# Kernel optimization log

Hardware: AMD Instinct MI355X
Metric: run time of the kernel (lower is better)

Reference implementation:

```python
import jax, jax.numpy as jnp
import numpy as np

B, LQ, LK = 1, 2048, 2048
D, H, KVH, DH = 4096, 32, 8, 128
G = H // KVH  # head groups


def setup_inputs() -> dict:
    key = jax.random.key(0)
    ks = jax.random.split(key, 7)
    s = 0.02
    hidden_q = jax.random.normal(ks[0], (B, LQ, D), dtype=jnp.float32)
    hidden_kv = jax.random.normal(ks[1], (B, LK, D), dtype=jnp.float32)
    # causal boolean mask (batch, len_q, len_k)
    attention_mask = jnp.broadcast_to(jnp.tril(jnp.ones((LQ, LK), dtype=bool)), (B, LQ, LK))
    position_bias = jax.random.normal(ks[2], (H, LQ, LK), dtype=jnp.float32) * 0.1
    Wq = jax.random.normal(ks[3], (D, H * DH), dtype=jnp.float32) * s
    Wk = jax.random.normal(ks[4], (D, KVH * DH), dtype=jnp.float32) * s
    Wv = jax.random.normal(ks[5], (D, KVH * DH), dtype=jnp.float32) * s
    Wo = jax.random.normal(ks[6], (H * DH, D), dtype=jnp.float32) * s
    return {"hidden_q": hidden_q, "hidden_kv": hidden_kv,
            "attention_mask": attention_mask, "position_bias": position_bias,
            "Wq": Wq, "Wk": Wk, "Wv": Wv, "Wo": Wo}


def reference(hidden_q, hidden_kv, attention_mask, position_bias, Wq, Wk, Wv, Wo):
    inv4 = DH ** -0.25  # q and k each scaled by dim_head**-1/4
    q = (hidden_q @ Wq) * inv4            # [B, LQ, H*DH]
    k = (hidden_kv @ Wk) * inv4           # [B, LK, KVH*DH]
    v = hidden_kv @ Wv                     # [B, LK, KVH*DH]
    q = q.reshape(B, LQ, KVH, G, DH)       # group heads for GQA
    k = k.reshape(B, LK, KVH, DH)
    v = v.reshape(B, LK, KVH, DH)
    # score: [B, KVH, G, LQ, LK] -> [B, H, LQ, LK]
    score = jnp.einsum('bqkgd,blkd->bkgql', q, k).reshape(B, H, LQ, LK)
    score = score + position_bias[None]
    mask = attention_mask[:, None]         # [B, 1, LQ, LK]
    score = jnp.where(mask, score, -jnp.inf)
    p = jax.nn.softmax(score, axis=-1)
    p = jnp.where(mask, p, 0.0)
    out = jnp.einsum('bkgql,blkd->bqkgd', p.reshape(B, KVH, G, LQ, LK), v)
    out = out.reshape(B, LQ, H * DH) @ Wo  # [B, LQ, D]
    return out
```

## Files before the change

### kernel.cpp

```cpp
#include <hip/hip_runtime.h>
#include <hip/hip_bf16.h>
#include <cstdint>
#include <cstddef>

typedef __attribute__((ext_vector_type(4))) float f32x4;
typedef __attribute__((ext_vector_type(4))) short s16x4;
typedef __attribute__((ext_vector_type(8))) short s16x8;

#define SLQ 2048
#define SLK 2048
#define SNH 32
#define SDH 128

__device__ __forceinline__ short f2bf(float x) {
  unsigned u = __builtin_bit_cast(unsigned, x);
  u += 0x7FFF + ((u >> 16) & 1);
  return (short)(u >> 16);
}

__device__ __forceinline__ void gload_lds16(const void* g, const void* l) {
  __builtin_amdgcn_global_load_lds((const __attribute__((address_space(1))) void*)g,
                                   (__attribute__((address_space(3))) void*)l,
                                   16, 0, 0);
}

template<int CTRL>
__device__ __forceinline__ float dpp_f32(float x) {
  return __builtin_bit_cast(float, __builtin_amdgcn_update_dpp(
      0, __builtin_bit_cast(int, x), CTRL, 0xF, 0xF, true));
}
__device__ __forceinline__ float rowmax16(float x) {
  x = fmaxf(x, dpp_f32<0x128>(x));
  x = fmaxf(x, dpp_f32<0x124>(x));
  x = fmaxf(x, dpp_f32<0x122>(x));
  x = fmaxf(x, dpp_f32<0x121>(x));
  return x;
}
__device__ __forceinline__ float rowsum16(float x) {
  x += dpp_f32<0x128>(x);
  x += dpp_f32<0x124>(x);
  x += dpp_f32<0x122>(x);
  x += dpp_f32<0x121>(x);
  return x;
}

__global__ void convert_bf16(const float* __restrict__ in, short* __restrict__ out, int n4) {
  int i = blockIdx.x * 256 + threadIdx.x;
  if (i < n4) {
    f32x4 a = ((const f32x4*)in)[i];
    s16x4 b;
    b[0] = f2bf(a[0]); b[1] = f2bf(a[1]); b[2] = f2bf(a[2]); b[3] = f2bf(a[3]);
    ((s16x4*)out)[i] = b;
  }
}

__global__ void transpose_convert(const float* __restrict__ W, short* __restrict__ Wt,
                                  int K, int N) {
  __shared__ short T[64][68];
  const int tid = threadIdx.x;
  const int k0 = blockIdx.y * 64, n0 = blockIdx.x * 64;
  const int r = tid >> 4;
  const int c4 = (tid & 15) * 4;
#pragma unroll
  for (int i = 0; i < 4; ++i) {
    f32x4 a = *(const f32x4*)(W + (size_t)(k0 + r + i * 16) * N + n0 + c4);
#pragma unroll
    for (int j = 0; j < 4; ++j) T[c4 + j][r + i * 16] = f2bf(a[j]);
  }
  __syncthreads();
  const int rn = tid >> 3;
  const int c8 = (tid & 7) * 8;
#pragma unroll
  for (int i = 0; i < 2; ++i) {
    s16x4 v0 = *(const s16x4*)&T[rn + i * 32][c8];
    s16x4 v1 = *(const s16x4*)&T[rn + i * 32][c8 + 4];
    short* dst = Wt + (size_t)(n0 + rn + i * 32) * K + k0 + c8;
    *(s16x4*)dst = v0;
    *(s16x4*)(dst + 4) = v1;
  }
}

template<int CM>
__global__ __launch_bounds__(512, 1)
void gemm_big(const short* __restrict__ A, const short* __restrict__ Bt,
              void* __restrict__ Cv, float scale) {
  __shared__ short As[3][128 * 64];
  __shared__ short Bs[3][256 * 64];
  const int N = 4096, K = 4096;
  const int tid = threadIdx.x, lane = tid & 63, w = tid >> 6;
  const int l15 = lane & 15, lg = lane >> 4;
  const int wr = w >> 2, wc = w & 3;
  const int nbx = N >> 8;
  const int nwg = gridDim.x, b = blockIdx.x;
  const int wg = (b & 7) * (nwg >> 3) + (b >> 3);
  const int m0 = (wg / nbx) * 128, n0 = (wg % nbx) * 256;

  f32x4 acc[4][4];
#pragma unroll
  for (int a = 0; a < 4; ++a)
#pragma unroll
    for (int c = 0; c < 4; ++c)
      acc[a][c] = (f32x4){0.f, 0.f, 0.f, 0.f};

#define GSTAGE(T, BUF) do {                                                    \
    _Pragma("unroll") for (int i_ = 0; i_ < 2; ++i_) {                         \
      const int ci = i_ * 512 + tid, r_ = ci >> 3, c_ = ci & 7;                \
      gload_lds16(A + (size_t)(m0 + r_) * K + (T) * 64 + ((c_ ^ (r_ & 7)) * 8),\
                  (const short*)As[BUF] + ci * 8); }                           \
    _Pragma("unroll") for (int i_ = 0; i_ < 4; ++i_) {                         \
      const int ci = i_ * 512 + tid, r_ = ci >> 3, c_ = ci & 7;                \
      gload_lds16(Bt + (size_t)(n0 + r_) * K + (T) * 64 + ((c_ ^ (r_ & 7)) * 8),\
                  (const short*)Bs[BUF] + ci * 8); }                           \
  } while (0)

  const int NT = K >> 6;
  GSTAGE(0, 0); GSTAGE(1, 1); GSTAGE(2, 2);
  int buf = 0;
  for (int t = 0; t < NT; ++t) {
    if (t + 2 < NT)      asm volatile("s_waitcnt vmcnt(12)" ::: "memory");
    else if (t + 1 < NT) asm volatile("s_waitcnt vmcnt(6)" ::: "memory");
    else                 asm volatile("s_waitcnt vmcnt(0)" ::: "memory");
    __builtin_amdgcn_s_barrier();
    const short* Ab = As[buf];
    const short* Bb = Bs[buf];
    s16x8 af[2][4], bfv[2][4];
#pragma unroll
    for (int kk = 0; kk < 2; ++kk) {
#pragma unroll
      for (int mi = 0; mi < 4; ++mi) {
        const int r = wr * 64 + mi * 16 + l15;
        const int c = (kk * 4 + lg) ^ (r & 7);
        af[kk][mi] = *(const s16x8*)(Ab + (r * 8 + c) * 8);
      }
#pragma unroll
      for (int ni = 0; ni < 4; ++ni) {
        const int r = wc * 64 + ni * 16 + l15;
        const int c = (kk * 4 + lg) ^ (r & 7);
        bfv[kk][ni] = *(const s16x8*)(Bb + (r * 8 + c) * 8);
      }
    }
    __builtin_amdgcn_s_setprio(1);
#pragma unroll
    for (int kk = 0; kk < 2; ++kk)
#pragma unroll
      for (int mi = 0; mi < 4; ++mi)
#pragma unroll
        for (int ni = 0; ni < 4; ++ni)
          acc[mi][ni] = __builtin_amdgcn_mfma_f32_16x16x32_bf16(af[kk][mi], bfv[kk][ni], acc[mi][ni], 0, 0, 0);
    __builtin_amdgcn_s_setprio(0);
    __builtin_amdgcn_s_barrier();
    if (t + 3 < NT) GSTAGE(t + 3, buf);
    buf = (buf == 2) ? 0 : buf + 1;
  }
#undef GSTAGE
#pragma unroll
  for (int mi = 0; mi < 4; ++mi) {
#pragma unroll
    for (int ni = 0; ni < 4; ++ni) {
#pragma unroll
      for (int j = 0; j < 4; ++j) {
        const int rg = m0 + wr * 64 + mi * 16 + lg * 4 + j;
        const int cg = n0 + wc * 64 + ni * 16 + l15;
        const float vv = acc[mi][ni][j] * scale;
        if (CM == 0) ((short*)Cv)[(size_t)rg * N + cg] = f2bf(vv);
        else         ((float*)Cv)[(size_t)rg * N + cg] = vv;
      }
    }
  }
}

__global__ __launch_bounds__(256, 2)
void gemm_kv(const short* __restrict__ A, const short* __restrict__ Bt,
             short* __restrict__ kout, short* __restrict__ vTout, float inv4) {
  __shared__ short As[128][32];
  __shared__ short Bs[128][32];
  const int N = 2048, K = 4096;
  const int tid = threadIdx.x, lane = tid & 63, wid = tid >> 6;
  const int l15 = lane & 15, lg = lane >> 4;
  const int nbx = N >> 7;
  const int nwg = gridDim.x, b = blockIdx.x;
  const int wg = (b & 7) * (nwg >> 3) + (b >> 3);
  const int m0 = (wg / nbx) * 128, n0 = (wg % nbx) * 128;
  const int wm = (wid >> 1) * 64, wn = (wid & 1) * 64;

  f32x4 acc[4][4];
#pragma unroll
  for (int a = 0; a < 4; ++a)
#pragma unroll
    for (int c = 0; c < 4; ++c)
      acc[a][c] = (f32x4){0.f, 0.f, 0.f, 0.f};

  for (int k0 = 0; k0 < K; k0 += 32) {
#pragma unroll
    for (int i = 0; i < 2; ++i) {
      const int c = i * 256 + wid * 64 + lane;
      const int rr = c >> 2, hh = (c & 3) * 8;
      gload_lds16(A  + (size_t)(m0 + rr) * K + k0 + hh,
                  (const short*)As + (size_t)(i * 256 + wid * 64) * 8);
      gload_lds16(Bt + (size_t)(n0 + rr) * K + k0 + hh,
                  (const short*)Bs + (size_t)(i * 256 + wid * 64) * 8);
    }
    __syncthreads();
    s16x8 af[4], bf[4];
#pragma unroll
    for (int mi = 0; mi < 4; ++mi)
      af[mi] = *(const s16x8*)&As[wm + mi * 16 + l15][lg * 8];
#pragma unroll
    for (int ni = 0; ni < 4; ++ni)
      bf[ni] = *(const s16x8*)&Bs[wn + ni * 16 + l15][lg * 8];
#pragma unroll
    for (int mi = 0; mi < 4; ++mi)
#pragma unroll
      for (int ni = 0; ni < 4; ++ni)
        acc[mi][ni] = __builtin_amdgcn_mfma_f32_16x16x32_bf16(af[mi], bf[ni], acc[mi][ni], 0, 0, 0);
    __syncthreads();
  }
  if (n0 < 1024) {
#pragma unroll
    for (int mi = 0; mi < 4; ++mi)
#pragma unroll
      for (int ni = 0; ni < 4; ++ni)
#pragma unroll
        for (int j = 0; j < 4; ++j) {
          const int rg = m0 + wm + mi * 16 + lg * 4 + j;
          const int cg = n0 + wn + ni * 16 + l15;
          kout[(size_t)rg * 1024 + cg] = f2bf(acc[mi][ni][j] * inv4);
        }
  } else {
#pragma unroll
    for (int mi = 0; mi < 4; ++mi)
#pragma unroll
      for (int ni = 0; ni < 4; ++ni) {
        s16x4 wv;
#pragma unroll
        for (int j = 0; j < 4; ++j) wv[j] = f2bf(acc[mi][ni][j]);
        const int rg0 = m0 + wm + mi * 16 + lg * 4;
        const int cg = n0 + wn + ni * 16 + l15 - 1024;
        *(s16x4*)(vTout + (size_t)cg * 2048 + rg0) = wv;
      }
  }
}

__global__ __launch_bounds__(256, 2)
void attn_kernel(const short* __restrict__ q, const short* __restrict__ k,
                 const short* __restrict__ vT, const float* __restrict__ bias,
                 short* __restrict__ o) {
  __shared__ __align__(16) short Ks[64 * 128];
  __shared__ __align__(16) short Vs[2][128 * 64];
  __shared__ __align__(16) short Ps[4][16][72];
  const int tid = threadIdx.x, lane = tid & 63, w = tid >> 6;
  const int l15 = lane & 15, lg = lane >> 4;
  const int b = blockIdx.x;
  const int h = b & 31;
  const int qt = 31 - (b >> 5);
  const int kvh = h >> 2;
  const int nt = qt + 1;

#define STAGE_K(IT) do { const int kv0_ = (IT) * 64;                          \
    _Pragma("unroll") for (int i_ = 0; i_ < 4; ++i_) {                        \
      const int ci = i_ * 256 + tid, r_ = ci >> 4, c_ = ci & 15;              \
      gload_lds16(k + (size_t)(kv0_ + r_) * 1024 + kvh * 128 + ((c_ ^ (r_ & 7)) * 8), \
                  (const short*)Ks + ci * 8); } } while (0)

#define STAGE_V(IT, P) do { const int kv0_ = (IT) * 64;                       \
    _Pragma("unroll") for (int i_ = 0; i_ < 4; ++i_) {                        \
      const int ci = i_ * 256 + tid, r_ = ci >> 3, c_ = ci & 7;               \
      gload_lds16(vT + (size_t)(kvh * 128 + r_) * 2048 + kv0_ + ((c_ ^ (r_ & 7)) * 8), \
                  (const short*)Vs[P] + ci * 8); } } while (0)

  const int qrow0 = qt * 64 + w * 16 + lg * 4;

  float bb[4][4];
#define LOAD_BIAS(IT) do { const float* bp_ = bias + ((size_t)h * SLQ + qrow0) * SLK + (IT) * 64 + l15; \
    _Pragma("unroll") for (int ni_ = 0; ni_ < 4; ++ni_)                       \
      _Pragma("unroll") for (int j_ = 0; j_ < 4; ++j_)                        \
        bb[ni_][j_] = bp_[(size_t)j_ * SLK + ni_ * 16]; } while (0)

  s16x8 qf[4];
  {
    const short* qp = q + (size_t)(qt * 64 + w * 16 + l15) * (SNH * SDH) + h * SDH + lg * 8;
#pragma unroll
    for (int kk = 0; kk < 4; ++kk) qf[kk] = *(const s16x8*)(qp + kk * 32);
  }
  float mrow[4], lrow[4];
  f32x4 oacc[8];
#pragma unroll
  for (int j = 0; j < 4; ++j) { mrow[j] = -1e30f; lrow[j] = 0.f; }
#pragma unroll
  for (int nd = 0; nd < 8; ++nd) oacc[nd] = (f32x4){0.f, 0.f, 0.f, 0.f};

  STAGE_V(0, 0);
  STAGE_K(0);
  LOAD_BIAS(0);

  for (int it = 0; it < nt; ++it) {
    const int p = it & 1;
    const int kv0 = it * 64;
    asm volatile("s_waitcnt vmcnt(16)" ::: "memory");
    __builtin_amdgcn_s_barrier();
    if (it + 1 < nt) STAGE_V(it + 1, p ^ 1);
    f32x4 s[4];
    __builtin_amdgcn_s_setprio(1);
#pragma unroll
    for (int ni = 0; ni < 4; ++ni) {
      s[ni] = (f32x4){0.f, 0.f, 0.f, 0.f};
      const int r = ni * 16 + l15;
#pragma unroll
      for (int kk = 0; kk < 4; ++kk) {
        const int cc = kk * 4 + lg;
        s16x8 kf = *(const s16x8*)(Ks + (r * 16 + (cc ^ (r & 7))) * 8);
        s[ni] = __builtin_amdgcn_mfma_f32_16x16x32_bf16(qf[kk], kf, s[ni], 0, 0, 0);
      }
    }
    __builtin_amdgcn_s_setprio(0);
#pragma unroll
    for (int ni = 0; ni < 4; ++ni) {
#pragma unroll
      for (int j = 0; j < 4; ++j) {
        float sv = s[ni][j] + bb[ni][j];
        if (it == qt && kv0 + ni * 16 + l15 > qrow0 + j) sv = -1e30f;
        s[ni][j] = sv;
      }
    }
    float pmax[4];
#pragma unroll
    for (int j = 0; j < 4; ++j) {
      float mx = fmaxf(fmaxf(s[0][j], s[1][j]), fmaxf(s[2][j], s[3][j]));
      pmax[j] = rowmax16(mx);
    }
    bool need = (pmax[0] > mrow[0] + 8.f) | (pmax[1] > mrow[1] + 8.f) |
                (pmax[2] > mrow[2] + 8.f) | (pmax[3] > mrow[3] + 8.f);
    if (__any(need)) {
#pragma unroll
      for (int j = 0; j < 4; ++j) {
        const float mn = fmaxf(mrow[j], pmax[j]);
        const float fsj = __expf(mrow[j] - mn);
        mrow[j] = mn;
        lrow[j] *= fsj;
#pragma unroll
        for (int nd = 0; nd < 8; ++nd) oacc[nd][j] *= fsj;
      }
    }
    float ps[4] = {0.f, 0.f, 0.f, 0.f};
#pragma unroll
    for (int ni = 0; ni < 4; ++ni)
#pragma unroll
      for (int j = 0; j < 4; ++j) {
        const float pv = __expf(s[ni][j] - mrow[j]);
        s[ni][j] = pv;
        ps[j] += pv;
      }
#pragma unroll
    for (int j = 0; j < 4; ++j) lrow[j] += rowsum16(ps[j]);
    __builtin_amdgcn_s_barrier();
    if (it + 1 < nt) { STAGE_K(it + 1); LOAD_BIAS(it + 1); }
#pragma unroll
    for (int ni = 0; ni < 4; ++ni)
#pragma unroll
      for (int j = 0; j < 4; ++j)
        Ps[w][lg * 4 + j][ni * 16 + l15] = f2bf(s[ni][j]);
    __builtin_amdgcn_s_setprio(1);
#pragma unroll
    for (int kk2 = 0; kk2 < 2; ++kk2) {
      s16x8 pa = *(const s16x8*)&Ps[w][l15][kk2 * 32 + lg * 8];
#pragma unroll
      for (int nd = 0; nd < 8; ++nd) {
        const int r = nd * 16 + l15;
        const int cc = kk2 * 4 + lg;
        s16x8 vf = *(const s16x8*)(Vs[p] + (r * 8 + (cc ^ (r & 7))) * 8);
        oacc[nd] = __builtin_amdgcn_mfma_f32_16x16x32_bf16(pa, vf, oacc[nd], 0, 0, 0);
      }
    }
    __builtin_amdgcn_s_setprio(0);
  }
#undef STAGE_K
#undef STAGE_V
#undef LOAD_BIAS
#pragma unroll
  for (int j = 0; j < 4; ++j) {
    const float inv = 1.f / lrow[j];
    short* op = o + (size_t)(qrow0 + j) * (SNH * SDH) + h * SDH + l15;
#pragma unroll
    for (int nd = 0; nd < 8; ++nd)
      op[nd * 16] = f2bf(oacc[nd][j] * inv);
  }
}

extern "C" void kernel_launch(void* const* d_in, const int* in_sizes, int n_in,
                              void* d_out, int out_size, void* d_ws, size_t ws_size,
                              hipStream_t stream) {
  (void)in_sizes; (void)n_in; (void)out_size; (void)ws_size;
  const float* hq   = (const float*)d_in[0];
  const float* hkv  = (const float*)d_in[1];
  const float* bias = (const float*)d_in[3];
  const float* Wq   = (const float*)d_in[4];
  const float* Wk   = (const float*)d_in[5];
  const float* Wv   = (const float*)d_in[6];
  const float* Wo   = (const float*)d_in[7];

  short* ws = (short*)d_ws;
  const size_t MEG = 1048576;
  short* hqb  = ws;
  short* hkvb = ws + 8 * MEG;
  short* WT   = ws + 16 * MEG;
  short* WkvT = ws + 32 * MEG;
  short* qb   = ws + 40 * MEG;
  short* kb   = ws + 48 * MEG;
  short* vbT  = ws + 50 * MEG;
  short* ob   = hqb;

  const float inv4 = 0.29730177875068026f;

  convert_bf16<<<8192, 256, 0, stream>>>(hq,  hqb,  2097152);
  convert_bf16<<<8192, 256, 0, stream>>>(hkv, hkvb, 2097152);

  transpose_convert<<<dim3(64, 64), 256, 0, stream>>>(Wq, WT, 4096, 4096);
  gemm_big<0><<<256, 512, 0, stream>>>(hqb, WT, qb, inv4);

  transpose_convert<<<dim3(16, 64), 256, 0, stream>>>(Wk, WkvT, 4096, 1024);
  transpose_convert<<<dim3(16, 64), 256, 0, stream>>>(Wv, WkvT + (size_t)1024 * 4096, 4096, 1024);
  gemm_kv<<<256, 256, 0, stream>>>(hkvb, WkvT, kb, vbT, inv4);

  attn_kernel<<<1024, 256, 0, stream>>>(qb, kb, vbT, bias, ob);

  transpose_convert<<<dim3(64, 64), 256, 0, stream>>>(Wo, WT, 4096, 4096);
  gemm_big<1><<<256, 512, 0, stream>>>(ob, WT, (float*)d_out, 1.0f);
}
```

Baseline: 425.9 us.

## Double-buffer K tiles, use exp2 softmax, and merge conversion/transpose launches

The attention kernel now double-buffers K in LDS so the next K and V tiles are staged right after the first barrier. This removes the second barrier per iteration, and the bias load is moved earlier. Softmax switches to exp2: log2(e) is folded into the Q projection scale and applied to the bias with an FMA, and the rescale threshold is widened to match. On the host side, the two conversions are fused into one launch and the four weight transposes into one, cutting launch count. The cost is more LDS, which may affect occupancy, plus a separate Wo buffer.

```diff
diff --git a/kernel.cpp b/kernel.cpp
--- a/kernel.cpp
+++ b/kernel.cpp
@@ -11,6 +11,7 @@
 #define SLK 2048
 #define SNH 32
 #define SDH 128
+#define LOG2E 1.4426950408889634f
 
 __device__ __forceinline__ short f2bf(float x) {
   unsigned u = __builtin_bit_cast(unsigned, x);
@@ -44,21 +45,31 @@
   return x;
 }
 
-__global__ void convert_bf16(const float* __restrict__ in, short* __restrict__ out, int n4) {
-  int i = blockIdx.x * 256 + threadIdx.x;
-  if (i < n4) {
-    f32x4 a = ((const f32x4*)in)[i];
-    s16x4 b;
-    b[0] = f2bf(a[0]); b[1] = f2bf(a[1]); b[2] = f2bf(a[2]); b[3] = f2bf(a[3]);
-    ((s16x4*)out)[i] = b;
-  }
-}
-
-__global__ void transpose_convert(const float* __restrict__ W, short* __restrict__ Wt,
-                                  int K, int N) {
+__global__ void convert_bf16_2(const float* __restrict__ in0, short* __restrict__ out0,
+                               const float* __restrict__ in1, short* __restrict__ out1) {
+  const int i = blockIdx.x * 256 + threadIdx.x;
+  const float* in = blockIdx.y ? in1 : in0;
+  short* out = blockIdx.y ? out1 : out0;
+  f32x4 a = ((const f32x4*)in)[i];
+  s16x4 b;
+  b[0] = f2bf(a[0]); b[1] = f2bf(a[1]); b[2] = f2bf(a[2]); b[3] = f2bf(a[3]);
+  ((s16x4*)out)[i] = b;
+}
+
+__global__ void transpose_all(const float* __restrict__ Wq, const float* __restrict__ Wo,
+                              const float* __restrict__ Wk, const float* __restrict__ Wv,
+                              short* __restrict__ WqT, short* __restrict__ WoT,
+                              short* __restrict__ WkT, short* __restrict__ WvT) {
   __shared__ short T[64][68];
+  const int K = 4096;
+  int bx = blockIdx.x;
+  const float* W; short* Wt; int N;
+  if (bx < 64)       { W = Wq; Wt = WqT; N = 4096; }
+  else if (bx < 128) { W = Wo; Wt = WoT; N = 4096; bx -= 64; }
+  else if (bx < 144) { W = Wk; Wt = WkT; N = 1024; bx -= 128; }
+  else               { W = Wv; Wt = WvT; N = 1024; bx -= 144; }
   const int tid = threadIdx.x;
-  const int k0 = blockIdx.y * 64, n0 = blockIdx.x * 64;
+  const int k0 = blockIdx.y * 64, n0 = bx * 64;
   const int r = tid >> 4;
   const int c4 = (tid & 15) * 4;
 #pragma unroll
@@ -245,7 +256,7 @@
 void attn_kernel(const short* __restrict__ q, const short* __restrict__ k,
                  const short* __restrict__ vT, const float* __restrict__ bias,
                  short* __restrict__ o) {
-  __shared__ __align__(16) short Ks[64 * 128];
+  __shared__ __align__(16) short Ks[2][64 * 128];
   __shared__ __align__(16) short Vs[2][128 * 64];
   __shared__ __align__(16) short Ps[4][16][72];
   const int tid = threadIdx.x, lane = tid & 63, w = tid >> 6;
@@ -256,11 +267,11 @@
   const int kvh = h >> 2;
   const int nt = qt + 1;
 
-#define STAGE_K(IT) do { const int kv0_ = (IT) * 64;                          \
+#define STAGE_K(IT, P) do { const int kv0_ = (IT) * 64;                       \
     _Pragma("unroll") for (int i_ = 0; i_ < 4; ++i_) {                        \
       const int ci = i_ * 256 + tid, r_ = ci >> 4, c_ = ci & 15;              \
       gload_lds16(k + (size_t)(kv0_ + r_) * 1024 + kvh * 128 + ((c_ ^ (r_ & 7)) * 8), \
-                  (const short*)Ks + ci * 8); } } while (0)
+                  (const short*)Ks[P] + ci * 8); } } while (0)
 
 #define STAGE_V(IT, P) do { const int kv0_ = (IT) * 64;                       \
     _Pragma("unroll") for (int i_ = 0; i_ < 4; ++i_) {                        \
@@ -290,7 +301,7 @@
   for (int nd = 0; nd < 8; ++nd) oacc[nd] = (f32x4){0.f, 0.f, 0.f, 0.f};
 
   STAGE_V(0, 0);
-  STAGE_K(0);
+  STAGE_K(0, 0);
   LOAD_BIAS(0);
 
   for (int it = 0; it < nt; ++it) {
@@ -298,7 +309,7 @@
     const int kv0 = it * 64;
     asm volatile("s_waitcnt vmcnt(16)" ::: "memory");
     __builtin_amdgcn_s_barrier();
-    if (it + 1 < nt) STAGE_V(it + 1, p ^ 1);
+    if (it + 1 < nt) { STAGE_V(it + 1, p ^ 1); STAGE_K(it + 1, p ^ 1); }
     f32x4 s[4];
     __builtin_amdgcn_s_setprio(1);
 #pragma unroll
@@ -308,7 +319,7 @@
 #pragma unroll
       for (int kk = 0; kk < 4; ++kk) {
         const int cc = kk * 4 + lg;
-        s16x8 kf = *(const s16x8*)(Ks + (r * 16 + (cc ^ (r & 7))) * 8);
+        s16x8 kf = *(const s16x8*)(Ks[p] + (r * 16 + (cc ^ (r & 7))) * 8);
         s[ni] = __builtin_amdgcn_mfma_f32_16x16x32_bf16(qf[kk], kf, s[ni], 0, 0, 0);
       }
     }
@@ -317,24 +328,25 @@
     for (int ni = 0; ni < 4; ++ni) {
 #pragma unroll
       for (int j = 0; j < 4; ++j) {
-        float sv = s[ni][j] + bb[ni][j];
+        float sv = fmaf(bb[ni][j], LOG2E, s[ni][j]);
         if (it == qt && kv0 + ni * 16 + l15 > qrow0 + j) sv = -1e30f;
         s[ni][j] = sv;
       }
     }
+    if (it + 1 < nt) LOAD_BIAS(it + 1);
     float pmax[4];
 #pragma unroll
     for (int j = 0; j < 4; ++j) {
       float mx = fmaxf(fmaxf(s[0][j], s[1][j]), fmaxf(s[2][j], s[3][j]));
       pmax[j] = rowmax16(mx);
     }
-    bool need = (pmax[0] > mrow[0] + 8.f) | (pmax[1] > mrow[1] + 8.f) |
-                (pmax[2] > mrow[2] + 8.f) | (pmax[3] > mrow[3] + 8.f);
+    bool need = (pmax[0] > mrow[0] + 11.54f) | (pmax[1] > mrow[1] + 11.54f) |
+                (pmax[2] > mrow[2] + 11.54f) | (pmax[3] > mrow[3] + 11.54f);
     if (__any(need)) {
 #pragma unroll
       for (int j = 0; j < 4; ++j) {
         const float mn = fmaxf(mrow[j], pmax[j]);
-        const float fsj = __expf(mrow[j] - mn);
+        const float fsj = exp2f(mrow[j] - mn);
         mrow[j] = mn;
         lrow[j] *= fsj;
 #pragma unroll
@@ -346,14 +358,12 @@
     for (int ni = 0; ni < 4; ++ni)
 #pragma unroll
       for (int j = 0; j < 4; ++j) {
-        const float pv = __expf(s[ni][j] - mrow[j]);
+        const float pv = exp2f(s[ni][j] - mrow[j]);
         s[ni][j] = pv;
         ps[j] += pv;
       }
 #pragma unroll
     for (int j = 0; j < 4; ++j) lrow[j] += rowsum16(ps[j]);
-    __builtin_amdgcn_s_barrier();
-    if (it + 1 < nt) { STAGE_K(it + 1); LOAD_BIAS(it + 1); }
 #pragma unroll
     for (int ni = 0; ni < 4; ++ni)
 #pragma unroll
@@ -403,26 +413,23 @@
   short* hqb  = ws;
   short* hkvb = ws + 8 * MEG;
   short* WT   = ws + 16 * MEG;
-  short* WkvT = ws + 32 * MEG;
-  short* qb   = ws + 40 * MEG;
-  short* kb   = ws + 48 * MEG;
-  short* vbT  = ws + 50 * MEG;
+  short* WoT  = ws + 32 * MEG;
+  short* WkvT = ws + 48 * MEG;
+  short* qb   = ws + 56 * MEG;
+  short* kb   = ws + 64 * MEG;
+  short* vbT  = ws + 66 * MEG;
   short* ob   = hqb;
 
   const float inv4 = 0.29730177875068026f;
 
-  convert_bf16<<<8192, 256, 0, stream>>>(hq,  hqb,  2097152);
-  convert_bf16<<<8192, 256, 0, stream>>>(hkv, hkvb, 2097152);
-
-  transpose_convert<<<dim3(64, 64), 256, 0, stream>>>(Wq, WT, 4096, 4096);
-  gemm_big<0><<<256, 512, 0, stream>>>(hqb, WT, qb, inv4);
-
-  transpose_convert<<<dim3(16, 64), 256, 0, stream>>>(Wk, WkvT, 4096, 1024);
-  transpose_convert<<<dim3(16, 64), 256, 0, stream>>>(Wv, WkvT + (size_t)1024 * 4096, 4096, 1024);
+  convert_bf16_2<<<dim3(8192, 2), 256, 0, stream>>>(hq, hqb, hkv, hkvb);
+  transpose_all<<<dim3(160, 64), 256, 0, stream>>>(
+      Wq, Wo, Wk, Wv, WT, WoT, WkvT, WkvT + (size_t)1024 * 4096);
+
+  gemm_big<0><<<256, 512, 0, stream>>>(hqb, WT, qb, inv4 * LOG2E);
   gemm_kv<<<256, 256, 0, stream>>>(hkvb, WkvT, kb, vbT, inv4);
 
   attn_kernel<<<1024, 256, 0, stream>>>(qb, kb, vbT, bias, ob);
 
-  transpose_convert<<<dim3(64, 64), 256, 0, stream>>>(Wo, WT, 4096, 4096);
-  gemm_big<1><<<256, 512, 0, stream>>>(ob, WT, (float*)d_out, 1.0f);
-}
+  gemm_big<1><<<256, 512, 0, stream>>>(ob, WoT, (float*)d_out, 1.0f);
+}
```

New measurement: 473.1 us. +11.1%, slower.
